# Optimization experiments

Measured on AMD Instinct MI355X. Metric: run time of the kernel, lower is better.

## Reference

```python
import jax, jax.numpy as jnp
import numpy as np

D_DEC, D_ENC, H, D_MLP = 1024, 768, 16, 4096
HD = D_DEC // H


def _layernorm(x, w, b, eps=1e-5):
    m = x.mean(-1, keepdims=True)
    v = ((x - m) ** 2).mean(-1, keepdims=True)
    return (x - m) / jnp.sqrt(v + eps) * w + b


def setup_inputs() -> dict:
    key = jax.random.key(0)
    ks = jax.random.split(key, 16)
    B, T, S = 4, 1024, 576

    def lin(k, din, dout):
        kw, kb = jax.random.split(k)
        bound = 1.0 / np.sqrt(din)
        W = jax.random.uniform(kw, (din, dout), jnp.float32, -bound, bound)
        b = jax.random.uniform(kb, (dout,), jnp.float32, -bound, bound)
        return W, b

    qkv_w, qkv_b = lin(ks[0], D_DEC, 3 * D_DEC)
    proj_w, proj_b = lin(ks[1], D_DEC, D_DEC)
    q_w, q_b = lin(ks[2], D_DEC, D_DEC)
    k_w, k_b = lin(ks[3], D_ENC, D_DEC)
    v_w, v_b = lin(ks[4], D_ENC, D_DEC)
    out_w, out_b = lin(ks[5], D_DEC, D_DEC)
    mlp1_w, mlp1_b = lin(ks[6], D_DEC, D_MLP)
    mlp2_w, mlp2_b = lin(ks[7], D_MLP, D_DEC)

    return {
        "x": jax.random.normal(ks[8], (B, T, D_DEC), jnp.float32),
        "enc": jax.random.normal(ks[9], (B, S, D_ENC), jnp.float32),
        "tgt_key_padding_mask": jnp.zeros((B, T), bool),
        "enc_padding_mask": jnp.zeros((B, S), bool),
        "ln1_w": jnp.ones((D_DEC,)), "ln1_b": jnp.zeros((D_DEC,)),
        "qkv_w": qkv_w, "qkv_b": qkv_b, "proj_w": proj_w, "proj_b": proj_b,
        "ln2_w": jnp.ones((D_DEC,)), "ln2_b": jnp.zeros((D_DEC,)),
        "q_w": q_w, "q_b": q_b, "k_w": k_w, "k_b": k_b,
        "v_w": v_w, "v_b": v_b, "out_w": out_w, "out_b": out_b,
        "ln3_w": jnp.ones((D_DEC,)), "ln3_b": jnp.zeros((D_DEC,)),
        "mlp1_w": mlp1_w, "mlp1_b": mlp1_b, "mlp2_w": mlp2_w, "mlp2_b": mlp2_b,
    }


def _decoder_block(x, enc, tgt_mask, enc_mask,
                   ln1_w, ln1_b, qkv_w, qkv_b, proj_w, proj_b,
                   ln2_w, ln2_b, q_w, q_b, k_w, k_b, v_w, v_b, out_w, out_b,
                   ln3_w, ln3_b, mlp1_w, mlp1_b, mlp2_w, mlp2_b):
    B, T, C = x.shape
    S = enc.shape[1]
    scale = HD ** -0.5
    neg = jnp.asarray(-jnp.inf, x.dtype)

    # ---- causal self-attention ----
    h = _layernorm(x, ln1_w, ln1_b)
    qkv = (h @ qkv_w + qkv_b).reshape(B, T, 3, H, HD)
    q, k, v = [qkv[:, :, i].transpose(0, 2, 1, 3) for i in range(3)]  # [B,H,T,HD]
    attn = jnp.einsum("bhtd,bhsd->bhts", q, k) * scale
    causal = jnp.triu(jnp.ones((T, T), bool), 1)
    attn = jnp.where(causal[None, None], neg, attn)
    attn = jnp.where(tgt_mask[:, None, None, :], neg, attn)
    attn = jax.nn.softmax(attn, axis=-1)
    sa = jnp.einsum("bhts,bhsd->bhtd", attn, v).transpose(0, 2, 1, 3).reshape(B, T, C)
    x = x + sa @ proj_w + proj_b

    # ---- cross-attention ----
    h = _layernorm(x, ln2_w, ln2_b)
    q = (h @ q_w + q_b).reshape(B, T, H, HD).transpose(0, 2, 1, 3)
    k = (enc @ k_w + k_b).reshape(B, S, H, HD).transpose(0, 2, 1, 3)
    v = (enc @ v_w + v_b).reshape(B, S, H, HD).transpose(0, 2, 1, 3)
    attn = jnp.einsum("bhtd,bhsd->bhts", q, k) * scale
    attn = jnp.where(enc_mask[:, None, None, :], neg, attn)
    attn = jax.nn.softmax(attn, axis=-1)
    ca = jnp.einsum("bhts,bhsd->bhtd", attn, v).transpose(0, 2, 1, 3).reshape(B, T, C)
    x = x + ca @ out_w + out_b

    # ---- MLP (exact GELU, matching torch nn.GELU default) ----
    h = _layernorm(x, ln3_w, ln3_b)
    h = jax.nn.gelu(h @ mlp1_w + mlp1_b, approximate=False)
    x = x + h @ mlp2_w + mlp2_b
    return x


def reference(x, enc, tgt_key_padding_mask, enc_padding_mask,
              ln1_w, ln1_b, qkv_w, qkv_b, proj_w, proj_b,
              ln2_w, ln2_b, q_w, q_b, k_w, k_b, v_w, v_b, out_w, out_b,
              ln3_w, ln3_b, mlp1_w, mlp1_b, mlp2_w, mlp2_b):
    return _decoder_block(x, enc, tgt_key_padding_mask, enc_padding_mask,
                          ln1_w, ln1_b, qkv_w, qkv_b, proj_w, proj_b,
                          ln2_w, ln2_b, q_w, q_b, k_w, k_b, v_w, v_b, out_w, out_b,
                          ln3_w, ln3_b, mlp1_w, mlp1_b, mlp2_w, mlp2_b)
```

## Files before the change

kernel.cpp:

```cpp
#include <hip/hip_runtime.h>
#include <hip/hip_bf16.h>

typedef unsigned short u16;
typedef __bf16 bf16x8 __attribute__((ext_vector_type(8)));
typedef float f32x4 __attribute__((ext_vector_type(4)));

__device__ __forceinline__ float bf2f(u16 v) { return __uint_as_float(((unsigned)v) << 16); }
__device__ __forceinline__ u16 f2bf(float f) {
  unsigned u = __float_as_uint(f);
  u += 0x7FFFu + ((u >> 16) & 1u);
  return (u16)(u >> 16);
}
__device__ __forceinline__ float gelu_exact(float x) {
  return 0.5f * x * (1.0f + erff(x * 0.70710678118654752f));
}

__device__ __forceinline__ void async_load16(const u16* g, u16* l) {
  __builtin_amdgcn_global_load_lds((const __attribute__((address_space(1))) void*)g,
                                   (__attribute__((address_space(3))) void*)l, 16, 0, 0);
}

__global__ void sniff_kernel(const u16* __restrict__ x, int* __restrict__ flag) {
  int tid = threadIdx.x;
  int hits = 0;
  #pragma unroll
  for (int s = 0; s < 2; ++s) {
    float f = fabsf(bf2f(x[2 * (tid + 64 * s)]));
    hits += (f >= 0.00390625f && f <= 16.0f) ? 1 : 0;
  }
  #pragma unroll
  for (int off = 32; off; off >>= 1) hits += __shfl_xor(hits, off);
  if (tid == 0) flag[0] = (hits >= 64) ? 1 : 0;
}

__global__ __launch_bounds__(256) void in2bf_kernel(const void* __restrict__ src, u16* __restrict__ dst,
                                                    int n4, const int* __restrict__ flagp) {
  int i = blockIdx.x * 256 + threadIdx.x;
  if (i >= n4) return;
  if (*flagp) {
    ((ushort4*)dst)[i] = ((const ushort4*)src)[i];
  } else {
    float4 v = ((const float4*)src)[i];
    ushort4 o; o.x = f2bf(v.x); o.y = f2bf(v.y); o.z = f2bf(v.z); o.w = f2bf(v.w);
    ((ushort4*)dst)[i] = o;
  }
}

__global__ __launch_bounds__(256) void small2bf_kernel(
    const void* s0, const void* s1, const void* s2, const void* s3,
    const void* s4, const void* s5, const void* s6, const void* s7,
    const void* s8, const void* s9, const void* s10, const void* s11,
    const void* s12, const void* s13,
    u16* __restrict__ dst, const int* __restrict__ flagp) {
  const void* srcs[14] = {s0, s1, s2, s3, s4, s5, s6, s7, s8, s9, s10, s11, s12, s13};
  int blk = blockIdx.x;
  int seg, u;
  if (blk < 6)       { seg = blk;            u = 0; }
  else if (blk < 9)  { seg = 6;              u = blk - 6; }
  else if (blk < 14) { seg = 7 + (blk - 9);  u = 0; }
  else if (blk < 18) { seg = 12;             u = blk - 14; }
  else               { seg = 13;             u = 0; }
  const void* src = srcs[seg];
  int i = threadIdx.x + u * 256;
  u16* d = dst + (size_t)blk * 1024;
  if (*flagp) {
    ((ushort4*)d)[threadIdx.x] = ((const ushort4*)src)[i];
  } else {
    float4 v = ((const float4*)src)[i];
    ushort4 o; o.x = f2bf(v.x); o.y = f2bf(v.y); o.z = f2bf(v.z); o.w = f2bf(v.w);
    ((ushort4*)d)[threadIdx.x] = o;
  }
}

__global__ __launch_bounds__(256) void in2f32_kernel(const void* __restrict__ src, float* __restrict__ dst,
                                                     int n4, const int* __restrict__ flagp) {
  int i = blockIdx.x * 256 + threadIdx.x;
  if (i >= n4) return;
  if (*flagp) {
    ushort4 v = ((const ushort4*)src)[i];
    float4 o; o.x = bf2f(v.x); o.y = bf2f(v.y); o.z = bf2f(v.z); o.w = bf2f(v.w);
    ((float4*)dst)[i] = o;
  } else {
    ((float4*)dst)[i] = ((const float4*)src)[i];
  }
}

__global__ __launch_bounds__(256) void transpose_k(const void* __restrict__ in_, u16* __restrict__ out,
                                                   int R, int C, const int* __restrict__ flagp) {
  int flag = *flagp;
  __shared__ u16 tile[32][33];
  int c0 = blockIdx.x * 32, r0 = blockIdx.y * 32;
  int tx = threadIdx.x & 31, ty = threadIdx.x >> 5;
  #pragma unroll
  for (int j = 0; j < 32; j += 8) {
    size_t idx = (size_t)(r0 + ty + j) * C + c0 + tx;
    tile[ty + j][tx] = flag ? ((const u16*)in_)[idx] : f2bf(((const float*)in_)[idx]);
  }
  __syncthreads();
  #pragma unroll
  for (int j = 0; j < 32; j += 8)
    out[(size_t)(c0 + ty + j) * R + r0 + tx] = tile[tx][ty + j];
}

__global__ __launch_bounds__(256) void ln_kernel(const float* __restrict__ x,
                                                 const u16* __restrict__ w, const u16* __restrict__ b,
                                                 u16* __restrict__ out) {
  int row = blockIdx.x, tid = threadIdx.x;
  float4 v = ((const float4*)(x + (size_t)row * 1024))[tid];
  float s = v.x + v.y + v.z + v.w;
  #pragma unroll
  for (int off = 32; off; off >>= 1) s += __shfl_xor(s, off);
  __shared__ float red1[4], red2[4];
  if ((tid & 63) == 0) red1[tid >> 6] = s;
  __syncthreads();
  float mean = (red1[0] + red1[1] + red1[2] + red1[3]) * (1.0f / 1024.0f);
  float d0 = v.x - mean, d1 = v.y - mean, d2 = v.z - mean, d3 = v.w - mean;
  float vs = d0 * d0 + d1 * d1 + d2 * d2 + d3 * d3;
  #pragma unroll
  for (int off = 32; off; off >>= 1) vs += __shfl_xor(vs, off);
  if ((tid & 63) == 0) red2[tid >> 6] = vs;
  __syncthreads();
  float var = (red2[0] + red2[1] + red2[2] + red2[3]) * (1.0f / 1024.0f);
  float rs = rsqrtf(var + 1e-5f);
  int c = tid * 4;
  ushort4 o;
  o.x = f2bf(d0 * rs * bf2f(w[c + 0]) + bf2f(b[c + 0]));
  o.y = f2bf(d1 * rs * bf2f(w[c + 1]) + bf2f(b[c + 1]));
  o.z = f2bf(d2 * rs * bf2f(w[c + 2]) + bf2f(b[c + 2]));
  o.w = f2bf(d3 * rs * bf2f(w[c + 3]) + bf2f(b[c + 3]));
  ((ushort4*)(out + (size_t)row * 1024))[tid] = o;
}

template <int MODE, int NB>
__global__ __launch_bounds__(256) void gemm_tn(const u16* __restrict__ A, const u16* __restrict__ Bt,
                                               const u16* __restrict__ bias,
                                               const float* __restrict__ resid_in, float* __restrict__ resid_out,
                                               void* __restrict__ outp, int M, int N, int K,
                                               const int* __restrict__ flagp) {
  __shared__ __align__(16) u16 As[NB][128 * 64];
  __shared__ __align__(16) u16 Bs[NB][128 * 64];
  int n0 = blockIdx.x * 128, m0 = blockIdx.y * 128;
  int tid = threadIdx.x;
  int lane = tid & 63, w = tid >> 6;
  int wm = w & 1, wn = w >> 1;
  int quad = lane >> 4, l15 = lane & 15;
  int sw = l15 & 7;
  int flag = (MODE == 3) ? *flagp : 0;
  f32x4 acc[4][4];
  #pragma unroll
  for (int i = 0; i < 4; i++)
    #pragma unroll
    for (int j = 0; j < 4; j++) acc[i][j] = (f32x4){0.f, 0.f, 0.f, 0.f};

  int srow8 = lane >> 3;
  int scol = ((lane & 7) ^ srow8) * 8;
  const u16* Abase = A + (size_t)(m0 + srow8) * K + scol;
  const u16* Bbase = Bt + (size_t)(n0 + srow8) * K + scol;

  auto issue = [&](int k0, int buf) {
    #pragma unroll
    for (int j = 0; j < 4; ++j) {
      int r0 = (w * 4 + j) * 8;
      async_load16(Abase + (size_t)r0 * K + k0, &As[buf][r0 * 64]);
      async_load16(Bbase + (size_t)r0 * K + k0, &Bs[buf][r0 * 64]);
    }
  };

  auto compute = [&](int buf) {
    #pragma unroll
    for (int kk = 0; kk < 64; kk += 32) {
      int cbase = (kk >> 3) + quad;
      int slot = (cbase ^ sw) << 3;
      bf16x8 af[4], bfr[4];
      #pragma unroll
      for (int i = 0; i < 4; i++) {
        af[i]  = *(const bf16x8*)&As[buf][(wm * 64 + i * 16 + l15) * 64 + slot];
        bfr[i] = *(const bf16x8*)&Bs[buf][(wn * 64 + i * 16 + l15) * 64 + slot];
      }
      #pragma unroll
      for (int mi = 0; mi < 4; mi++)
        #pragma unroll
        for (int ni = 0; ni < 4; ni++)
          acc[mi][ni] = __builtin_amdgcn_mfma_f32_16x16x32_bf16(af[mi], bfr[ni], acc[mi][ni], 0, 0, 0);
    }
  };

  if (NB == 3) {
    int nt = K >> 6;
    issue(0, 0);
    if (nt > 1) issue(64, 1);
    int cur = 0;
    for (int t = 0; t < nt; ++t) {
      if (t + 1 < nt) { asm volatile("s_waitcnt vmcnt(8)" ::: "memory"); }
      else            { asm volatile("s_waitcnt vmcnt(0)" ::: "memory"); }
      __builtin_amdgcn_s_barrier();
      if (t + 2 < nt) {
        int nb = cur + 2; if (nb >= 3) nb -= 3;
        issue((t + 2) << 6, nb);
      }
      compute(cur);
      if (++cur == 3) cur = 0;
    }
  } else {
    for (int k0 = 0; k0 < K; k0 += 64) {
      issue(k0, 0);
      __syncthreads();
      compute(0);
      __syncthreads();
    }
  }

  int col_base = n0 + wn * 64, row_base = m0 + wm * 64;
  #pragma unroll
  for (int mi = 0; mi < 4; mi++) {
    #pragma unroll
    for (int ni = 0; ni < 4; ni++) {
      int col = col_base + ni * 16 + l15;
      float bv = bf2f(bias[col]);
      #pragma unroll
      for (int r = 0; r < 4; r++) {
        int row = row_base + mi * 16 + quad * 4 + r;
        float vv = acc[mi][ni][r] + bv;
        size_t idx = (size_t)row * N + col;
        if (MODE == 0) ((u16*)outp)[idx] = f2bf(vv);
        else if (MODE == 1) resid_out[idx] = resid_in[idx] + vv;
        else if (MODE == 2) ((u16*)outp)[idx] = f2bf(gelu_exact(vv));
        else {
          float ov = resid_in[idx] + vv;
          if (flag) ((u16*)outp)[idx] = f2bf(ov);
          else ((float*)outp)[idx] = ov;
        }
      }
    }
  }
}

__global__ __launch_bounds__(256) void attn_mfma(const u16* __restrict__ Q, const u16* __restrict__ K,
                                                 const u16* __restrict__ V, u16* __restrict__ O,
                                                 int T, int S, int qstride, int kstride, int causal) {
  int bh = blockIdx.y, b = bh >> 4, h = bh & 15;
  const u16* Qb = Q + (size_t)b * T * qstride + h * 64;
  const u16* Kb = K + (size_t)b * S * kstride + h * 64;
  const u16* Vb = V + (size_t)b * S * kstride + h * 64;
  u16* Ob = O + (size_t)b * T * 1024 + h * 64;

  int tid = threadIdx.x, lane = tid & 63, w = tid >> 6;
  int quad = lane >> 4, l15 = lane & 15;
  int qt = blockIdx.x * 64;

  __shared__ __align__(16) u16 Ks[64 * 72];
  __shared__ __align__(16) u16 Vt[64 * 72];
  __shared__ __align__(16) u16 Ps[4][16 * 72];

  int sr = tid >> 2, sc0 = (tid & 3) * 16;

  *(uint4*)&Ks[sr * 72 + sc0]     = *(const uint4*)&Qb[(size_t)(qt + sr) * qstride + sc0];
  *(uint4*)&Ks[sr * 72 + sc0 + 8] = *(const uint4*)&Qb[(size_t)(qt + sr) * qstride + sc0 + 8];
  __syncthreads();
  bf16x8 qfrag[2];
  #pragma unroll
  for (int c = 0; c < 2; ++c)
    qfrag[c] = *(const bf16x8*)&Ks[(w * 16 + l15) * 72 + c * 32 + quad * 8];

  float m_i[4], l_i[4];
  f32x4 oacc[4];
  #pragma unroll
  for (int r = 0; r < 4; ++r) { m_i[r] = -1e30f; l_i[r] = 0.f; }
  #pragma unroll
  for (int ni = 0; ni < 4; ++ni) oacc[ni] = (f32x4){0.f, 0.f, 0.f, 0.f};

  int nk = causal ? (blockIdx.x + 1) * 64 : S;
  int tg0 = qt + w * 16 + quad * 4;

  for (int s0 = 0; s0 < nk; s0 += 64) {
    __syncthreads();
    *(uint4*)&Ks[sr * 72 + sc0]     = *(const uint4*)&Kb[(size_t)(s0 + sr) * kstride + sc0];
    *(uint4*)&Ks[sr * 72 + sc0 + 8] = *(const uint4*)&Kb[(size_t)(s0 + sr) * kstride + sc0 + 8];
    uint4 v0 = *(const uint4*)&Vb[(size_t)(s0 + sr) * kstride + sc0];
    uint4 v1 = *(const uint4*)&Vb[(size_t)(s0 + sr) * kstride + sc0 + 8];
    union { uint4 u[2]; u16 e[16]; } vv; vv.u[0] = v0; vv.u[1] = v1;
    #pragma unroll
    for (int j = 0; j < 16; ++j) Vt[(sc0 + j) * 72 + sr] = vv.e[j];
    __syncthreads();

    f32x4 sacc[4];
    #pragma unroll
    for (int ni = 0; ni < 4; ++ni) sacc[ni] = (f32x4){0.f, 0.f, 0.f, 0.f};
    #pragma unroll
    for (int c = 0; c < 2; ++c) {
      #pragma unroll
      for (int ni = 0; ni < 4; ++ni) {
        bf16x8 kf = *(const bf16x8*)&Ks[(ni * 16 + l15) * 72 + c * 32 + quad * 8];
        sacc[ni] = __builtin_amdgcn_mfma_f32_16x16x32_bf16(qfrag[c], kf, sacc[ni], 0, 0, 0);
      }
    }

    #pragma unroll
    for (int ni = 0; ni < 4; ++ni) {
      int key = s0 + ni * 16 + l15;
      #pragma unroll
      for (int r = 0; r < 4; ++r) {
        float sv = sacc[ni][r] * 0.125f;
        if (causal && key > tg0 + r) sv = -1e30f;
        sacc[ni][r] = sv;
      }
    }

    float mnew[4], alpha[4], psum[4];
    #pragma unroll
    for (int r = 0; r < 4; ++r) {
      float mx = fmaxf(fmaxf(sacc[0][r], sacc[1][r]), fmaxf(sacc[2][r], sacc[3][r]));
      #pragma unroll
      for (int off = 1; off < 16; off <<= 1) mx = fmaxf(mx, __shfl_xor(mx, off));
      mnew[r] = fmaxf(m_i[r], mx);
      alpha[r] = __expf(m_i[r] - mnew[r]);
      m_i[r] = mnew[r];
      psum[r] = 0.f;
    }
    #pragma unroll
    for (int ni = 0; ni < 4; ++ni) {
      #pragma unroll
      for (int r = 0; r < 4; ++r) {
        float p = __expf(sacc[ni][r] - mnew[r]);
        psum[r] += p;
        Ps[w][(quad * 4 + r) * 72 + ni * 16 + l15] = f2bf(p);
      }
    }
    #pragma unroll
    for (int r = 0; r < 4; ++r) {
      float ps = psum[r];
      #pragma unroll
      for (int off = 1; off < 16; off <<= 1) ps += __shfl_xor(ps, off);
      l_i[r] = l_i[r] * alpha[r] + ps;
    }

    bf16x8 pfrag[2];
    #pragma unroll
    for (int c = 0; c < 2; ++c)
      pfrag[c] = *(const bf16x8*)&Ps[w][l15 * 72 + c * 32 + quad * 8];

    #pragma unroll
    for (int ni = 0; ni < 4; ++ni)
      #pragma unroll
      for (int r = 0; r < 4; ++r) oacc[ni][r] *= alpha[r];
    #pragma unroll
    for (int c = 0; c < 2; ++c) {
      #pragma unroll
      for (int ni = 0; ni < 4; ++ni) {
        bf16x8 vf = *(const bf16x8*)&Vt[(ni * 16 + l15) * 72 + c * 32 + quad * 8];
        oacc[ni] = __builtin_amdgcn_mfma_f32_16x16x32_bf16(pfrag[c], vf, oacc[ni], 0, 0, 0);
      }
    }
  }

  #pragma unroll
  for (int ni = 0; ni < 4; ++ni) {
    #pragma unroll
    for (int r = 0; r < 4; ++r) {
      int t = tg0 + r;
      int d = ni * 16 + l15;
      Ob[(size_t)t * 1024 + d] = f2bf(oacc[ni][r] / l_i[r]);
    }
  }
}

extern "C" void kernel_launch(void* const* d_in, const int* in_sizes, int n_in,
                              void* d_out, int out_size, void* d_ws, size_t ws_size,
                              hipStream_t stream) {
  const void* x_in   = d_in[0];
  const void* enc_in = d_in[1];
  const void* ln1_w = d_in[4];  const void* ln1_b = d_in[5];
  const void* qkv_w = d_in[6];  const void* qkv_b = d_in[7];
  const void* proj_w = d_in[8]; const void* proj_b = d_in[9];
  const void* ln2_w = d_in[10]; const void* ln2_b = d_in[11];
  const void* q_w = d_in[12];   const void* q_b = d_in[13];
  const void* k_w = d_in[14];   const void* k_b = d_in[15];
  const void* v_w = d_in[16];   const void* v_b = d_in[17];
  const void* out_w = d_in[18]; const void* out_b = d_in[19];
  const void* ln3_w = d_in[20]; const void* ln3_b = d_in[21];
  const void* mlp1_w = d_in[22]; const void* mlp1_b = d_in[23];
  const void* mlp2_w = d_in[24]; const void* mlp2_b = d_in[25];

  char* ws = (char*)d_ws;
  size_t off = 0;
  auto alloc = [&](size_t bytes) { char* p = ws + off; off += (bytes + 255) & ~(size_t)255; return p; };
  float* xf   = (float*)alloc(4096ull * 1024 * 4);
  u16* hb     = (u16*)alloc(4096ull * 1024 * 2);
  u16* big    = (u16*)alloc(4096ull * 4096 * 2);
  u16* wT     = (u16*)alloc(3072ull * 1024 * 2);
  u16* encb   = (u16*)alloc(2304ull * 768 * 2);
  u16* pool   = (u16*)alloc(20480ull * 2);
  int* flag   = (int*)alloc(256);
  (void)ws_size;

  u16* q_bf = big;
  u16* k_bf = big + 4096ull * 1024;
  u16* v_bf = big + (4096ull + 2304) * 1024;

  u16 *p_ln1w = pool, *p_ln1b = pool + 1024, *p_ln2w = pool + 2048, *p_ln2b = pool + 3072;
  u16 *p_ln3w = pool + 4096, *p_ln3b = pool + 5120;
  u16 *p_qkvb = pool + 6144, *p_projb = pool + 9216, *p_qb = pool + 10240, *p_kb = pool + 11264;
  u16 *p_vb = pool + 12288, *p_outb = pool + 13312, *p_m1b = pool + 14336, *p_m2b = pool + 18432;

  sniff_kernel<<<1, 64, 0, stream>>>((const u16*)x_in, flag);
  in2f32_kernel<<<4096, 256, 0, stream>>>(x_in, xf, 1048576, flag);
  in2bf_kernel<<<1728, 256, 0, stream>>>(enc_in, encb, 442368, flag);
  small2bf_kernel<<<19, 256, 0, stream>>>(ln1_w, ln1_b, ln2_w, ln2_b, ln3_w, ln3_b,
                                          qkv_b, proj_b, q_b, k_b, v_b, out_b,
                                          mlp1_b, mlp2_b, pool, flag);

  ln_kernel<<<4096, 256, 0, stream>>>(xf, p_ln1w, p_ln1b, hb);
  transpose_k<<<dim3(96, 32), 256, 0, stream>>>(qkv_w, wT, 1024, 3072, flag);
  gemm_tn<0, 1><<<dim3(24, 32), 256, 0, stream>>>(hb, wT, p_qkvb, nullptr, nullptr, big, 4096, 3072, 1024, flag);
  attn_mfma<<<dim3(16, 64), 256, 0, stream>>>(big, big + 1024, big + 2048, hb, 1024, 1024, 3072, 3072, 1);
  transpose_k<<<dim3(32, 32), 256, 0, stream>>>(proj_w, wT, 1024, 1024, flag);
  gemm_tn<1, 3><<<dim3(8, 32), 256, 0, stream>>>(hb, wT, p_projb, xf, xf, nullptr, 4096, 1024, 1024, flag);

  ln_kernel<<<4096, 256, 0, stream>>>(xf, p_ln2w, p_ln2b, hb);
  transpose_k<<<dim3(32, 32), 256, 0, stream>>>(q_w, wT, 1024, 1024, flag);
  gemm_tn<0, 3><<<dim3(8, 32), 256, 0, stream>>>(hb, wT, p_qb, nullptr, nullptr, q_bf, 4096, 1024, 1024, flag);
  transpose_k<<<dim3(32, 24), 256, 0, stream>>>(k_w, wT, 768, 1024, flag);
  gemm_tn<0, 3><<<dim3(8, 18), 256, 0, stream>>>(encb, wT, p_kb, nullptr, nullptr, k_bf, 2304, 1024, 768, flag);
  transpose_k<<<dim3(32, 24), 256, 0, stream>>>(v_w, wT, 768, 1024, flag);
  gemm_tn<0, 3><<<dim3(8, 18), 256, 0, stream>>>(encb, wT, p_vb, nullptr, nullptr, v_bf, 2304, 1024, 768, flag);
  attn_mfma<<<dim3(16, 64), 256, 0, stream>>>(q_bf, k_bf, v_bf, hb, 1024, 576, 1024, 1024, 0);
  transpose_k<<<dim3(32, 32), 256, 0, stream>>>(out_w, wT, 1024, 1024, flag);
  gemm_tn<1, 3><<<dim3(8, 32), 256, 0, stream>>>(hb, wT, p_outb, xf, xf, nullptr, 4096, 1024, 1024, flag);

  ln_kernel<<<4096, 256, 0, stream>>>(xf, p_ln3w, p_ln3b, hb);
  transpose_k<<<dim3(128, 32), 256, 0, stream>>>(mlp1_w, wT, 1024, 4096, flag);
  gemm_tn<2, 1><<<dim3(32, 32), 256, 0, stream>>>(hb, wT, p_m1b, nullptr, nullptr, big, 4096, 4096, 1024, flag);
  transpose_k<<<dim3(32, 128), 256, 0, stream>>>(mlp2_w, wT, 4096, 1024, flag);
  gemm_tn<3, 3><<<dim3(8, 32), 256, 0, stream>>>(big, wT, p_m2b, xf, nullptr, d_out, 4096, 1024, 4096, flag);
}
```

Baseline: 611.8 us.

## Use 128x64 tiles for N=1024 GEMMs, drop triple buffering, add XCD-aware block remap

The GEMM template now takes an N-tile width instead of a buffer count. The N=1024 GEMMs use 128x64 tiles, which doubles the grid to about 512 blocks and gives the 256 CUs more parallel work. The triple-buffered async pipeline is removed in favour of a simple single-buffer load/sync/compute loop that uses less LDS. Block IDs are also remapped in chunks of eight so that neighbouring tiles land on the same XCD and share L2. The cost is lost overlap between loads and MFMA compute, plus less operand reuse per block.

```diff
diff --git a/kernel.cpp b/kernel.cpp
--- a/kernel.cpp
+++ b/kernel.cpp
@@ -131,90 +131,77 @@
   ((ushort4*)(out + (size_t)row * 1024))[tid] = o;
 }
 
-template <int MODE, int NB>
+template <int MODE, int TN>
 __global__ __launch_bounds__(256) void gemm_tn(const u16* __restrict__ A, const u16* __restrict__ Bt,
                                                const u16* __restrict__ bias,
                                                const float* __restrict__ resid_in, float* __restrict__ resid_out,
                                                void* __restrict__ outp, int M, int N, int K,
                                                const int* __restrict__ flagp) {
-  __shared__ __align__(16) u16 As[NB][128 * 64];
-  __shared__ __align__(16) u16 Bs[NB][128 * 64];
-  int n0 = blockIdx.x * 128, m0 = blockIdx.y * 128;
+  constexpr int NI = TN / 32;
+  __shared__ __align__(16) u16 As[128 * 64];
+  __shared__ __align__(16) u16 Bs[TN * 64];
+
+  int nwg = gridDim.x * gridDim.y;
+  int bid = blockIdx.y * gridDim.x + blockIdx.x;
+  int chunk = nwg >> 3;
+  int s = (bid & 7) * chunk + (bid >> 3);
+  int bx = s % gridDim.x, by = s / gridDim.x;
+
+  int n0 = bx * TN, m0 = by * 128;
   int tid = threadIdx.x;
   int lane = tid & 63, w = tid >> 6;
   int wm = w & 1, wn = w >> 1;
   int quad = lane >> 4, l15 = lane & 15;
   int sw = l15 & 7;
   int flag = (MODE == 3) ? *flagp : 0;
-  f32x4 acc[4][4];
+  f32x4 acc[4][NI];
   #pragma unroll
   for (int i = 0; i < 4; i++)
     #pragma unroll
-    for (int j = 0; j < 4; j++) acc[i][j] = (f32x4){0.f, 0.f, 0.f, 0.f};
+    for (int j = 0; j < NI; j++) acc[i][j] = (f32x4){0.f, 0.f, 0.f, 0.f};
 
   int srow8 = lane >> 3;
   int scol = ((lane & 7) ^ srow8) * 8;
   const u16* Abase = A + (size_t)(m0 + srow8) * K + scol;
   const u16* Bbase = Bt + (size_t)(n0 + srow8) * K + scol;
 
-  auto issue = [&](int k0, int buf) {
+  for (int k0 = 0; k0 < K; k0 += 64) {
     #pragma unroll
     for (int j = 0; j < 4; ++j) {
       int r0 = (w * 4 + j) * 8;
-      async_load16(Abase + (size_t)r0 * K + k0, &As[buf][r0 * 64]);
-      async_load16(Bbase + (size_t)r0 * K + k0, &Bs[buf][r0 * 64]);
-    }
-  };
-
-  auto compute = [&](int buf) {
+      async_load16(Abase + (size_t)r0 * K + k0, &As[r0 * 64]);
+    }
+    #pragma unroll
+    for (int j = 0; j < TN / 32; ++j) {
+      int r0 = (w * (TN / 32) + j) * 8;
+      async_load16(Bbase + (size_t)r0 * K + k0, &Bs[r0 * 64]);
+    }
+    __syncthreads();
     #pragma unroll
     for (int kk = 0; kk < 64; kk += 32) {
       int cbase = (kk >> 3) + quad;
       int slot = (cbase ^ sw) << 3;
-      bf16x8 af[4], bfr[4];
-      #pragma unroll
-      for (int i = 0; i < 4; i++) {
-        af[i]  = *(const bf16x8*)&As[buf][(wm * 64 + i * 16 + l15) * 64 + slot];
-        bfr[i] = *(const bf16x8*)&Bs[buf][(wn * 64 + i * 16 + l15) * 64 + slot];
-      }
+      bf16x8 af[4], bfr[NI];
+      #pragma unroll
+      for (int i = 0; i < 4; i++)
+        af[i] = *(const bf16x8*)&As[(wm * 64 + i * 16 + l15) * 64 + slot];
+      #pragma unroll
+      for (int j = 0; j < NI; j++)
+        bfr[j] = *(const bf16x8*)&Bs[(wn * (TN / 2) + j * 16 + l15) * 64 + slot];
       #pragma unroll
       for (int mi = 0; mi < 4; mi++)
         #pragma unroll
-        for (int ni = 0; ni < 4; ni++)
+        for (int ni = 0; ni < NI; ni++)
           acc[mi][ni] = __builtin_amdgcn_mfma_f32_16x16x32_bf16(af[mi], bfr[ni], acc[mi][ni], 0, 0, 0);
     }
-  };
-
-  if (NB == 3) {
-    int nt = K >> 6;
-    issue(0, 0);
-    if (nt > 1) issue(64, 1);
-    int cur = 0;
-    for (int t = 0; t < nt; ++t) {
-      if (t + 1 < nt) { asm volatile("s_waitcnt vmcnt(8)" ::: "memory"); }
-      else            { asm volatile("s_waitcnt vmcnt(0)" ::: "memory"); }
-      __builtin_amdgcn_s_barrier();
-      if (t + 2 < nt) {
-        int nb = cur + 2; if (nb >= 3) nb -= 3;
-        issue((t + 2) << 6, nb);
-      }
-      compute(cur);
-      if (++cur == 3) cur = 0;
-    }
-  } else {
-    for (int k0 = 0; k0 < K; k0 += 64) {
-      issue(k0, 0);
-      __syncthreads();
-      compute(0);
-      __syncthreads();
-    }
-  }
-
-  int col_base = n0 + wn * 64, row_base = m0 + wm * 64;
+    __syncthreads();
+  }
+
+  int col_base = n0 + wn * (TN / 2), row_base = m0 + wm * 64;
   #pragma unroll
   for (int mi = 0; mi < 4; mi++) {
     #pragma unroll
-    for (int ni = 0; ni < 4; ni++) {
+    for (int ni = 0; ni < NI; ni++) {
       int col = col_base + ni * 16 + l15;
       float bv = bf2f(bias[col]);
       #pragma unroll
@@ -411,25 +398,25 @@
 
   ln_kernel<<<4096, 256, 0, stream>>>(xf, p_ln1w, p_ln1b, hb);
   transpose_k<<<dim3(96, 32), 256, 0, stream>>>(qkv_w, wT, 1024, 3072, flag);
-  gemm_tn<0, 1><<<dim3(24, 32), 256, 0, stream>>>(hb, wT, p_qkvb, nullptr, nullptr, big, 4096, 3072, 1024, flag);
+  gemm_tn<0, 128><<<dim3(24, 32), 256, 0, stream>>>(hb, wT, p_qkvb, nullptr, nullptr, big, 4096, 3072, 1024, flag);
   attn_mfma<<<dim3(16, 64), 256, 0, stream>>>(big, big + 1024, big + 2048, hb, 1024, 1024, 3072, 3072, 1);
   transpose_k<<<dim3(32, 32), 256, 0, stream>>>(proj_w, wT, 1024, 1024, flag);
-  gemm_tn<1, 3><<<dim3(8, 32), 256, 0, stream>>>(hb, wT, p_projb, xf, xf, nullptr, 4096, 1024, 1024, flag);
+  gemm_tn<1, 64><<<dim3(16, 32), 256, 0, stream>>>(hb, wT, p_projb, xf, xf, nullptr, 4096, 1024, 1024, flag);
 
   ln_kernel<<<4096, 256, 0, stream>>>(xf, p_ln2w, p_ln2b, hb);
   transpose_k<<<dim3(32, 32), 256, 0, stream>>>(q_w, wT, 1024, 1024, flag);
-  gemm_tn<0, 3><<<dim3(8, 32), 256, 0, stream>>>(hb, wT, p_qb, nullptr, nullptr, q_bf, 4096, 1024, 1024, flag);
+  gemm_tn<0, 64><<<dim3(16, 32), 256, 0, stream>>>(hb, wT, p_qb, nullptr, nullptr, q_bf, 4096, 1024, 1024, flag);
   transpose_k<<<dim3(32, 24), 256, 0, stream>>>(k_w, wT, 768, 1024, flag);
-  gemm_tn<0, 3><<<dim3(8, 18), 256, 0, stream>>>(encb, wT, p_kb, nullptr, nullptr, k_bf, 2304, 1024, 768, flag);
+  gemm_tn<0, 64><<<dim3(16, 18), 256, 0, stream>>>(encb, wT, p_kb, nullptr, nullptr, k_bf, 2304, 1024, 768, flag);
   transpose_k<<<dim3(32, 24), 256, 0, stream>>>(v_w, wT, 768, 1024, flag);
-  gemm_tn<0, 3><<<dim3(8, 18), 256, 0, stream>>>(encb, wT, p_vb, nullptr, nullptr, v_bf, 2304, 1024, 768, flag);
+  gemm_tn<0, 64><<<dim3(16, 18), 256, 0, stream>>>(encb, wT, p_vb, nullptr, nullptr, v_bf, 2304, 1024, 768, flag);
   attn_mfma<<<dim3(16, 64), 256, 0, stream>>>(q_bf, k_bf, v_bf, hb, 1024, 576, 1024, 1024, 0);
   transpose_k<<<dim3(32, 32), 256, 0, stream>>>(out_w, wT, 1024, 1024, flag);
-  gemm_tn<1, 3><<<dim3(8, 32), 256, 0, stream>>>(hb, wT, p_outb, xf, xf, nullptr, 4096, 1024, 1024, flag);
+  gemm_tn<1, 64><<<dim3(16, 32), 256, 0, stream>>>(hb, wT, p_outb, xf, xf, nullptr, 4096, 1024, 1024, flag);
 
   ln_kernel<<<4096, 256, 0, stream>>>(xf, p_ln3w, p_ln3b, hb);
   transpose_k<<<dim3(128, 32), 256, 0, stream>>>(mlp1_w, wT, 1024, 4096, flag);
-  gemm_tn<2, 1><<<dim3(32, 32), 256, 0, stream>>>(hb, wT, p_m1b, nullptr, nullptr, big, 4096, 4096, 1024, flag);
+  gemm_tn<2, 128><<<dim3(32, 32), 256, 0, stream>>>(hb, wT, p_m1b, nullptr, nullptr, big, 4096, 4096, 1024, flag);
   transpose_k<<<dim3(32, 128), 256, 0, stream>>>(mlp2_w, wT, 4096, 1024, flag);
-  gemm_tn<3, 3><<<dim3(8, 32), 256, 0, stream>>>(big, wT, p_m2b, xf, nullptr, d_out, 4096, 1024, 4096, flag);
-}
+  gemm_tn<3, 64><<<dim3(16, 32), 256, 0, stream>>>(big, wT, p_m2b, xf, nullptr, d_out, 4096, 1024, 4096, flag);
+}
```

Measured after the change: 595.7 us. -2.6%, faster.
